# Kernel tuning notes

Measured on AMD Instinct MI355X. Metric: run time of the kernel, lower is better.

## Reference

```python
import jax, jax.numpy as jnp
import numpy as np

ALPHA = 1.0
EPS = 1e-6

NUM_CLASSES = 100000
FEAT_DIM = 256
BATCH = 8192


def setup_inputs() -> dict:
    key = jax.random.key(0)
    k1, k2 = jax.random.split(key)
    features = jax.random.normal(k1, (BATCH, FEAT_DIM), dtype=jnp.float32)
    target = jax.random.randint(k2, (BATCH,), 0, NUM_CLASSES, dtype=jnp.int64)
    # centers bank initialized to zeros as in the torch module
    centers = jnp.zeros((NUM_CLASSES, FEAT_DIM), dtype=jnp.float32)
    return {"features": features, "target": target, "centers": centers}


def reference(features, target, centers):
    # gather per-sample class centers: [B, D]
    centers_batch = centers[target]
    # MSE loss over all elements (nn.MSELoss default reduction='mean')
    diff = centers_batch - features  # [B, D]
    center_loss = jnp.mean(diff * diff)
    # per-class appearance counts, gathered back per sample
    counts = jax.ops.segment_sum(
        jnp.ones((target.shape[0],), dtype=jnp.float32), target,
        num_segments=NUM_CLASSES)  # [C]
    appear = counts[target]  # [B]
    # per-sample scaled update, scatter-added into the centers bank
    upd = ALPHA * diff / (appear + EPS)[:, None]  # [B, D]
    delta = jax.ops.segment_sum(upd, target, num_segments=NUM_CLASSES)  # [C, D]
    new_centers = centers - delta
    return center_loss, new_centers
```

## Files before the change

### kernel.cpp

```cpp
#include <hip/hip_runtime.h>

#define BATCH   8192
#define FEAT    256
#define NCLASS  100000
#define EPS_C   1e-6f

#define NC_ELEMS (NCLASS * FEAT)
#define NVEC (NC_ELEMS / 4)
#define FUSED_BLOCKS (NVEC / 256)

__global__ void build_kernel(const int* __restrict__ target,
                             int* __restrict__ head,
                             int* __restrict__ next) {
    int b = blockIdx.x * blockDim.x + threadIdx.x;
    if (b < BATCH) next[b] = atomicExch(&head[target[b]], b);
}

__global__ void fused_kernel(const float* __restrict__ centers,
                             const float* __restrict__ features,
                             const int* __restrict__ head,
                             const int* __restrict__ next,
                             float* __restrict__ partials,
                             float* __restrict__ out ) {
    int w = threadIdx.x >> 6;
    int l = threadIdx.x & 63;
    int r = blockIdx.x * 4 + w;

    const float4 c4 = ((const float4*)(centers + (size_t)r * FEAT))[l];
    float4 n4 = c4;
    int h = head[r];
    if (h != -1) {
        float4 sumf = {0.f, 0.f, 0.f, 0.f};
        int n = 0;
        for (int s = h; s != -1; s = next[s]) {
            float4 f4 = ((const float4*)(features + (size_t)s * FEAT))[l];
            sumf.x += f4.x; sumf.y += f4.y; sumf.z += f4.z; sumf.w += f4.w;
            float dx = c4.x - f4.x, dy = c4.y - f4.y;
            float dz = c4.z - f4.z, dw = c4.w - f4.w;
            float sq = dx*dx + dy*dy + dz*dz + dw*dw;
            #pragma unroll
            for (int off = 32; off > 0; off >>= 1) sq += __shfl_down(sq, off, 64);
            if (l == 0) partials[s] = sq;
            n++;
        }
        float nf = (float)n;
        float inv = 1.0f / (nf + EPS_C);
        n4.x = c4.x - (nf * c4.x - sumf.x) * inv;
        n4.y = c4.y - (nf * c4.y - sumf.y) * inv;
        n4.z = c4.z - (nf * c4.z - sumf.z) * inv;
        n4.w = c4.w - (nf * c4.w - sumf.w) * inv;
    }

    float pw = __shfl_up(n4.w, 1, 64);
    if (l > 0) {
        float4 ov = {pw, n4.x, n4.y, n4.z};
        ((float4*)out)[(size_t)r * 64 + l];
        ((float4*)out)[(size_t)r * 64 + l] = ov;
    } else {
        size_t base = (size_t)r * FEAT;
        out[base + 1] = n4.x;
        out[base + 2] = n4.y;
        out[base + 3] = n4.z;
    }
    if (l == 63) {
        out[(size_t)(r + 1) * FEAT] = n4.w;
    }
}

__global__ void finalize_kernel(const float* __restrict__ partials,
                                float* __restrict__ out0) {
    float s = 0.0f;
    for (int i = threadIdx.x; i < BATCH; i += 256) s += partials[i];
    #pragma unroll
    for (int off = 32; off > 0; off >>= 1) s += __shfl_down(s, off, 64);
    __shared__ float red[4];
    int wave = threadIdx.x >> 6;
    int lane = threadIdx.x & 63;
    if (lane == 0) red[wave] = s;
    __syncthreads();
    if (threadIdx.x == 0) {
        out0[0] = (red[0] + red[1] + red[2] + red[3]) / (float)(BATCH * FEAT);
    }
}

extern "C" void kernel_launch(void* const* d_in, const int* in_sizes, int n_in,
                              void* d_out, int out_size, void* d_ws, size_t ws_size,
                              hipStream_t stream) {
    const float* features = (const float*)d_in[0];
    const int*   target   = (const int*)d_in[1];
    const float* centers  = (const float*)d_in[2];
    float* out = (float*)d_out;

    int*   head     = (int*)d_ws;
    int*   next     = head + NCLASS;
    float* partials = (float*)(next + BATCH);

    hipMemsetAsync(head, 0xFF, NCLASS * sizeof(int), stream);
    build_kernel<<<(BATCH + 255) / 256, 256, 0, stream>>>(target, head, next);
    fused_kernel<<<FUSED_BLOCKS, 256, 0, stream>>>(centers, features, head, next,
                                                   partials, out);
    finalize_kernel<<<1, 256, 0, stream>>>(partials, out);
}
```

Before: 201.4 us.

## Process four center rows per wave and use unaligned vector stores for output

Each wave now handles four consecutive class rows instead of one. It loads all four center rows and head pointers up front so that more memory requests are in flight, and the block count drops fourfold. The shuffle-based realignment of the output, which is offset by one float for the loss scalar, is replaced with a direct unaligned 16-byte store. This removes the cross-lane shuffle and the split edge stores, but the unaligned vector writes may be split by hardware and register pressure rises.

```diff
diff --git a/kernel.cpp b/kernel.cpp
--- a/kernel.cpp
+++ b/kernel.cpp
@@ -6,8 +6,12 @@
 #define EPS_C   1e-6f
 
 #define NC_ELEMS (NCLASS * FEAT)
-#define NVEC (NC_ELEMS / 4)
-#define FUSED_BLOCKS (NVEC / 256)
+#define ROWS_PER_WAVE 4
+#define ROWS_PER_BLOCK 16
+#define FUSED_BLOCKS (NCLASS / ROWS_PER_BLOCK)
+
+typedef float float4a __attribute__((vector_size(16)));
+typedef float4a float4u __attribute__((aligned(4)));
 
 __global__ void build_kernel(const int* __restrict__ target,
                              int* __restrict__ head,
@@ -24,46 +28,50 @@
                              float* __restrict__ out ) {
     int w = threadIdx.x >> 6;
     int l = threadIdx.x & 63;
-    int r = blockIdx.x * 4 + w;
+    int rb = blockIdx.x * ROWS_PER_BLOCK + w * ROWS_PER_WAVE;
 
-    const float4 c4 = ((const float4*)(centers + (size_t)r * FEAT))[l];
-    float4 n4 = c4;
-    int h = head[r];
-    if (h != -1) {
-        float4 sumf = {0.f, 0.f, 0.f, 0.f};
-        int n = 0;
-        for (int s = h; s != -1; s = next[s]) {
-            float4 f4 = ((const float4*)(features + (size_t)s * FEAT))[l];
-            sumf.x += f4.x; sumf.y += f4.y; sumf.z += f4.z; sumf.w += f4.w;
-            float dx = c4.x - f4.x, dy = c4.y - f4.y;
-            float dz = c4.z - f4.z, dw = c4.w - f4.w;
-            float sq = dx*dx + dy*dy + dz*dz + dw*dw;
-            #pragma unroll
-            for (int off = 32; off > 0; off >>= 1) sq += __shfl_down(sq, off, 64);
-            if (l == 0) partials[s] = sq;
-            n++;
+    const float4* cb = (const float4*)centers;
+    float4 c0 = cb[(size_t)(rb + 0) * 64 + l];
+    float4 c1 = cb[(size_t)(rb + 1) * 64 + l];
+    float4 c2 = cb[(size_t)(rb + 2) * 64 + l];
+    float4 c3 = cb[(size_t)(rb + 3) * 64 + l];
+    int h0 = head[rb + 0];
+    int h1 = head[rb + 1];
+    int h2 = head[rb + 2];
+    int h3 = head[rb + 3];
+
+    float4 c[4] = {c0, c1, c2, c3};
+    int    h[4] = {h0, h1, h2, h3};
+
+    #pragma unroll
+    for (int j = 0; j < ROWS_PER_WAVE; ++j) {
+        int r = rb + j;
+        float4 c4 = c[j];
+        float4 n4 = c4;
+        if (h[j] != -1) {
+            float4 sumf = {0.f, 0.f, 0.f, 0.f};
+            int n = 0;
+            for (int s = h[j]; s != -1; s = next[s]) {
+                float4 f4 = ((const float4*)(features + (size_t)s * FEAT))[l];
+                sumf.x += f4.x; sumf.y += f4.y; sumf.z += f4.z; sumf.w += f4.w;
+                float dx = c4.x - f4.x, dy = c4.y - f4.y;
+                float dz = c4.z - f4.z, dw = c4.w - f4.w;
+                float sq = dx*dx + dy*dy + dz*dz + dw*dw;
+                #pragma unroll
+                for (int off = 32; off > 0; off >>= 1)
+                    sq += __shfl_down(sq, off, 64);
+                if (l == 0) partials[s] = sq;
+                n++;
+            }
+            float nf = (float)n;
+            float inv = 1.0f / (nf + EPS_C);
+            n4.x = c4.x - (nf * c4.x - sumf.x) * inv;
+            n4.y = c4.y - (nf * c4.y - sumf.y) * inv;
+            n4.z = c4.z - (nf * c4.z - sumf.z) * inv;
+            n4.w = c4.w - (nf * c4.w - sumf.w) * inv;
         }
-        float nf = (float)n;
-        float inv = 1.0f / (nf + EPS_C);
-        n4.x = c4.x - (nf * c4.x - sumf.x) * inv;
-        n4.y = c4.y - (nf * c4.y - sumf.y) * inv;
-        n4.z = c4.z - (nf * c4.z - sumf.z) * inv;
-        n4.w = c4.w - (nf * c4.w - sumf.w) * inv;
-    }
-
-    float pw = __shfl_up(n4.w, 1, 64);
-    if (l > 0) {
-        float4 ov = {pw, n4.x, n4.y, n4.z};
-        ((float4*)out)[(size_t)r * 64 + l];
-        ((float4*)out)[(size_t)r * 64 + l] = ov;
-    } else {
-        size_t base = (size_t)r * FEAT;
-        out[base + 1] = n4.x;
-        out[base + 2] = n4.y;
-        out[base + 3] = n4.z;
-    }
-    if (l == 63) {
-        out[(size_t)(r + 1) * FEAT] = n4.w;
+        *(float4u*)(out + 1 + (size_t)r * FEAT + 4 * l) =
+            (float4u){n4.x, n4.y, n4.z, n4.w};
     }
 }
 
```

Measured after the change: 209.0 us. 3.8% more time.
